# Kernel tuning notes

Measured on AMD Instinct MI355X. Metric: run time of the kernel, lower is better.

## Reference

```python
import jax, jax.numpy as jnp
import numpy as np

N = 200000      # nodes (1000 graphs x 200 nodes)
E = 1600000     # edges
N1 = 100000     # nodes after pool 1
E2 = 100000     # edges of pooled graph
N2 = 50000      # nodes after pool 2
B = 1000        # graphs
F_IN, C1, C2, H, NCLS = 1, 32, 64, 25, 10


def setup_inputs() -> dict:
    key = jax.random.key(0)
    ks = jax.random.split(key, 16)
    def lin(k, i, o):
        return jax.random.normal(k, (i, o), jnp.float32) / np.sqrt(i)
    inp = {
        'x': jax.random.normal(ks[0], (N, F_IN), jnp.float32),
        'pos': jax.random.uniform(ks[1], (N, 2), jnp.float32),
        'edge_index': jax.random.randint(ks[2], (2, E), 0, N, dtype=jnp.int32),
        'edge_attr': jax.random.uniform(ks[3], (E, 2), jnp.float32),
        'batch': (jnp.arange(N, dtype=jnp.int32) // (N // B)),
        'cluster1': (jnp.arange(N, dtype=jnp.int32) // 2),      # pairs of consecutive nodes -> same graph
        'edge_index2': jax.random.randint(ks[4], (2, E2), 0, N1, dtype=jnp.int32),
        'cluster2': (jnp.arange(N1, dtype=jnp.int32) // 2),
        'n1_w1': lin(ks[5], 2, H), 'n1_b1': jnp.zeros((H,), jnp.float32),
        'n1_w2': lin(ks[6], H, F_IN * C1), 'n1_b2': jnp.zeros((F_IN * C1,), jnp.float32),
        'root1': lin(ks[7], F_IN, C1), 'bias1': jnp.zeros((C1,), jnp.float32),
        'n2_w1': lin(ks[8], 2, H), 'n2_b1': jnp.zeros((H,), jnp.float32),
        'n2_w2': lin(ks[9], H, C1 * C2), 'n2_b2': jnp.zeros((C1 * C2,), jnp.float32),
        'root2': lin(ks[10], C1, C2), 'bias2': jnp.zeros((C2,), jnp.float32),
        'fc1_w': lin(ks[11], C2, 128), 'fc1_b': jnp.zeros((128,), jnp.float32),
        'fc2_w': lin(ks[12], 128, NCLS), 'fc2_b': jnp.zeros((NCLS,), jnp.float32),
    }
    return inp


def _cartesian(ei, pos):
    # PyG transforms.Cartesian(norm=True, cat=False)
    cart = pos[ei[0]] - pos[ei[1]]                      # [E, 2]
    m = jnp.max(jnp.abs(cart))
    return cart / (2.0 * m) + 0.5


def _nnconv(x, ei, ea, w1, b1, w2, b2, root, bias, n_nodes, c_in, c_out):
    # edge-conditioned weights: MLP(edge_attr) -> [E, c_in, c_out]
    w = (jax.nn.relu(ea @ w1 + b1) @ w2 + b2).reshape(-1, c_in, c_out)
    msg = jnp.einsum('ei,eio->eo', x[ei[0]], w)          # per-edge matmul with gathered src feats
    agg = jax.ops.segment_sum(msg, ei[1], num_segments=n_nodes)
    return agg + x @ root + bias


def _segment_mean(v, seg, n):
    s = jax.ops.segment_sum(v, seg, num_segments=n)
    c = jax.ops.segment_sum(jnp.ones((v.shape[0], 1), v.dtype), seg, num_segments=n)
    return s / jnp.maximum(c, 1.0)


def reference(x, pos, edge_index, edge_attr, batch, cluster1, edge_index2, cluster2,
              n1_w1, n1_b1, n1_w2, n1_b2, root1, bias1,
              n2_w1, n2_b1, n2_w2, n2_b2, root2, bias2,
              fc1_w, fc1_b, fc2_w, fc2_b):
    h = jax.nn.elu(_nnconv(x, edge_index, edge_attr, n1_w1, n1_b1, n1_w2, n1_b2,
                           root1, bias1, N, F_IN, C1))
    # max_pool(cluster1): segment-max feats, mean pos, carry batch; recompute Cartesian attrs
    x1 = jax.ops.segment_max(h, cluster1, num_segments=N1)
    pos1 = _segment_mean(pos, cluster1, N1)
    batch1 = jax.ops.segment_max(batch, cluster1, num_segments=N1)
    ea2 = _cartesian(edge_index2, pos1)
    h2 = jax.nn.elu(_nnconv(x1, edge_index2, ea2, n2_w1, n2_b1, n2_w2, n2_b2,
                            root2, bias2, N1, C1, C2))
    # max_pool_x(cluster2)
    x2 = jax.ops.segment_max(h2, cluster2, num_segments=N2)
    batch2 = jax.ops.segment_max(batch1, cluster2, num_segments=N2)
    g = _segment_mean(x2, batch2, B)                    # global_mean_pool -> [B, 64]
    z = jax.nn.elu(g @ fc1_w + fc1_b)                   # dropout is identity in eval
    return jax.nn.log_softmax(z @ fc2_w + fc2_b, axis=1)
```

## Files before the change

kernel.cpp:

```cpp
#include <hip/hip_runtime.h>
#include <hip/hip_bf16.h>

#define N_NODES 200000
#define E1 1600000
#define N1P 100000
#define E2P 100000
#define N2P 50000
#define BGR 1000
#define C1 32
#define C2 64
#define HIDN 25
#define NCLS 10

typedef short short8 __attribute__((ext_vector_type(8)));
typedef int int4v __attribute__((ext_vector_type(4)));
typedef float f32x4 __attribute__((ext_vector_type(4)));
typedef float f32x2 __attribute__((ext_vector_type(2)));

union FragU { int4v i; short8 s; };

__device__ __forceinline__ float elu1(float v) {
    return v > 0.f ? v : expm1f(v);
}
__device__ __forceinline__ float bf2f(unsigned short u) {
    return __uint_as_float(((unsigned int)u) << 16);
}
__device__ __forceinline__ unsigned int pk_bf16(float a, float b) {
    unsigned int r;
    asm("v_cvt_pk_bf16_f32 %0, %1, %2" : "=v"(r) : "v"(a), "v"(b));
    return r;
}
__device__ __forceinline__ void atomic_pk_bf16(unsigned short* p, unsigned int pk) {
    asm volatile("global_atomic_pk_add_bf16 %0, %1, off" :: "v"(p), "v"(pk) : "memory");
}

__global__ __launch_bounds__(256) void bgbuild1_kernel(
    const float* __restrict__ w2, const float* __restrict__ b2,
    unsigned int* __restrict__ W2f)
{
    int q = blockIdx.x * 256 + threadIdx.x;
    if (q >= 512) return;
    int jj = q & 3, l = (q >> 2) & 63, m = q >> 8;
    int k0 = (l >> 4) * 8 + 2 * jj;
    int o = 2 * (l & 15) + m;
    float v0 = (k0 < 25) ? w2[k0 * 32 + o] : (k0 == 25 ? b2[o] : 0.f);
    int k1 = k0 + 1;
    float v1 = (k1 < 25) ? w2[k1 * 32 + o] : (k1 == 25 ? b2[o] : 0.f);
    W2f[q] = pk_bf16(v0, v1);
}

__global__ __launch_bounds__(256) void conv1_kernel(
    const float* __restrict__ x, const float* __restrict__ ea,
    const int* __restrict__ ei,
    const float* __restrict__ w1, const float* __restrict__ b1,
    const unsigned int* __restrict__ W2f,
    unsigned short* __restrict__ agg1b)
{
    __shared__ unsigned int afrag[16][4][64];
    __shared__ int dst_lds[256];

    int t = threadIdx.x;
    int e = blockIdx.x * 256 + t;
    f32x2 a = ((const f32x2*)ea)[e];
    int s = ei[e], d = ei[E1 + e];
    float xv = x[s];
    dst_lds[t] = d;

    float v[26];
#pragma unroll
    for (int h = 0; h < HIDN; ++h) {
        float u = fmaf(a.x, w1[h], fmaf(a.y, w1[HIDN + h], b1[h]));
        v[h] = fmaxf(u, 0.f) * xv;
    }
    v[25] = xv;

    int tile = t >> 4, r = t & 15;
#pragma unroll
    for (int p = 0; p < 13; ++p) {
        int g = p >> 2, j = p & 3;
        afrag[tile][j][g * 16 + r] = pk_bf16(v[2 * p], v[2 * p + 1]);
    }
    afrag[tile][1][48 + r] = 0;
    afrag[tile][2][48 + r] = 0;
    afrag[tile][3][48 + r] = 0;
    __syncthreads();

    int lane = t & 63, wave = t >> 6;
    FragU bf0, bf1;
    bf0.i = *(const int4v*)(W2f + lane * 4);
    bf1.i = *(const int4v*)(W2f + (64 + lane) * 4);
    int c = lane & 15, rg = lane >> 4;

#pragma unroll
    for (int ti = 0; ti < 4; ++ti) {
        int tl = wave * 4 + ti;
        FragU af;
        af.i.x = afrag[tl][0][lane];
        af.i.y = afrag[tl][1][lane];
        af.i.z = afrag[tl][2][lane];
        af.i.w = afrag[tl][3][lane];
        f32x4 a0 = (f32x4){0.f, 0.f, 0.f, 0.f};
        f32x4 a1 = (f32x4){0.f, 0.f, 0.f, 0.f};
        a0 = __builtin_amdgcn_mfma_f32_16x16x32_bf16(af.s, bf0.s, a0, 0, 0, 0);
        a1 = __builtin_amdgcn_mfma_f32_16x16x32_bf16(af.s, bf1.s, a1, 0, 0, 0);
#pragma unroll
        for (int jj = 0; jj < 4; ++jj) {
            int le = tl * 16 + rg * 4 + jj;
            atomic_pk_bf16(agg1b + (size_t)dst_lds[le] * C1 + 2 * c,
                           pk_bf16(a0[jj], a1[jj]));
        }
    }
}

__global__ __launch_bounds__(256) void pool1_kernel(
    const unsigned short* __restrict__ agg1b, const float* __restrict__ x,
    const float* __restrict__ root1, const float* __restrict__ bias1,
    const float* __restrict__ pos, unsigned short* __restrict__ x1b,
    float* __restrict__ pos1)
{
    int t = blockIdx.x * blockDim.x + threadIdx.x;
    if (t >= N1P * C1) return;
    int j = t >> 5, o = t & 31;
    int na = 2 * j, nb = 2 * j + 1;
    float r = root1[o], bo = bias1[o];
    float ha = elu1(bf2f(agg1b[(size_t)na * C1 + o]) + x[na] * r + bo);
    float hb = elu1(bf2f(agg1b[(size_t)nb * C1 + o]) + x[nb] * r + bo);
    float mx = fmaxf(ha, hb);
    x1b[t] = (unsigned short)(pk_bf16(mx, mx) & 0xffffu);
    if (o < 2) pos1[j * 2 + o] = 0.5f * (pos[na * 2 + o] + pos[nb * 2 + o]);
}

__global__ __launch_bounds__(256) void maxabs_kernel(
    const int* __restrict__ ei2, const float* __restrict__ pos1,
    unsigned int* __restrict__ maxbits)
{
    int e = blockIdx.x * blockDim.x + threadIdx.x;
    float m = 0.f;
    if (e < E2P) {
        int s = ei2[e], d = ei2[E2P + e];
        float c0 = pos1[2 * s] - pos1[2 * d];
        float c1 = pos1[2 * s + 1] - pos1[2 * d + 1];
        m = fmaxf(fabsf(c0), fabsf(c1));
    }
#pragma unroll
    for (int off = 32; off; off >>= 1)
        m = fmaxf(m, __shfl_down(m, off));
    if ((threadIdx.x & 63) == 0)
        atomicMax(maxbits, __float_as_uint(m));
}

__global__ __launch_bounds__(256) void bgbuild_kernel(
    const float* __restrict__ w2, const float* __restrict__ b2,
    unsigned int* __restrict__ Bg)
{
    int idx = blockIdx.x * 256 + threadIdx.x;
    if (idx >= 26 * 4 * 64 * 4) return;
    int g0 = idx * 2;
    int j = g0 & 7;
    int l = (g0 >> 3) & 63;
    int nb = (g0 >> 9) & 3;
    int kt = g0 >> 11;
    int k = kt * 32 + (l >> 4) * 8 + j;
    int o = (nb >> 1) * 32 + 2 * (l & 15) + (nb & 1);
    float v0, v1;
    if (k < 800) { v0 = w2[k * 64 + o]; v1 = w2[(k + 1) * 64 + o]; }
    else         { v0 = b2[(k - 800) * 64 + o]; v1 = b2[(k - 799) * 64 + o]; }
    Bg[idx] = pk_bf16(v0, v1);
}

__global__ __launch_bounds__(256) void conv2_kernel(
    const int* __restrict__ ei2, const float* __restrict__ pos1,
    const unsigned short* __restrict__ x1b,
    const float* __restrict__ w1, const float* __restrict__ b1,
    const unsigned int* __restrict__ maxbits,
    const unsigned int* __restrict__ Bg,
    unsigned short* __restrict__ agg2b)
{
    __shared__ __align__(16) unsigned short xs_lds[256][40];
    __shared__ float hid_lds[256][27];
    __shared__ int dst_lds[256];

    int t = threadIdx.x;
    int ge = blockIdx.x * 256 + t;

    {
        float inv = 0.5f / __uint_as_float(maxbits[0]);
        int s = 0, d = 0;
        if (ge < E2P) { s = ei2[ge]; d = ei2[E2P + ge]; }
        dst_lds[t] = d;
        float a0 = (pos1[2 * s] - pos1[2 * d]) * inv + 0.5f;
        float a1 = (pos1[2 * s + 1] - pos1[2 * d + 1]) * inv + 0.5f;
#pragma unroll
        for (int h = 0; h < HIDN; ++h) {
            float u = fmaf(a0, w1[h], fmaf(a1, w1[HIDN + h], b1[h]));
            hid_lds[t][h] = fmaxf(u, 0.f);
        }
        const int4v* xp = (const int4v*)(x1b + (size_t)s * C1);
#pragma unroll
        for (int q = 0; q < 4; ++q)
            *(int4v*)&xs_lds[t][q * 8] = xp[q];
    }
    __syncthreads();

    int lane = t & 63, wave = t >> 6;
    int c = lane & 15, rg = lane >> 4;

    FragU xv4[4];
    float xfl[4][8];
#pragma unroll
    for (int ti = 0; ti < 4; ++ti) {
        int row = (wave * 4 + ti) * 16 + c;
        xv4[ti].i = *(const int4v*)&xs_lds[row][rg * 8];
#pragma unroll
        for (int g2 = 0; g2 < 4; ++g2) {
            unsigned int u = (unsigned int)xv4[ti].i[g2];
            xfl[ti][2 * g2]     = __uint_as_float(u << 16);
            xfl[ti][2 * g2 + 1] = __uint_as_float(u & 0xffff0000u);
        }
    }

    f32x4 acc[4][4];
#pragma unroll
    for (int ti = 0; ti < 4; ++ti)
#pragma unroll
        for (int nb = 0; nb < 4; ++nb)
            acc[ti][nb] = (f32x4){0.f, 0.f, 0.f, 0.f};

    const int4v* Bg4 = (const int4v*)Bg;
#pragma unroll 2
    for (int kt = 0; kt < 25; ++kt) {
        FragU bf[4];
#pragma unroll
        for (int nb = 0; nb < 4; ++nb)
            bf[nb].i = Bg4[(kt * 4 + nb) * 64 + lane];
#pragma unroll
        for (int ti = 0; ti < 4; ++ti) {
            float hv = hid_lds[(wave * 4 + ti) * 16 + c][kt];
            FragU af;
            af.i.x = pk_bf16(hv * xfl[ti][0], hv * xfl[ti][1]);
            af.i.y = pk_bf16(hv * xfl[ti][2], hv * xfl[ti][3]);
            af.i.z = pk_bf16(hv * xfl[ti][4], hv * xfl[ti][5]);
            af.i.w = pk_bf16(hv * xfl[ti][6], hv * xfl[ti][7]);
#pragma unroll
            for (int nb = 0; nb < 4; ++nb)
                acc[ti][nb] = __builtin_amdgcn_mfma_f32_16x16x32_bf16(af.s, bf[nb].s, acc[ti][nb], 0, 0, 0);
        }
    }
    {
        FragU bf[4];
#pragma unroll
        for (int nb = 0; nb < 4; ++nb)
            bf[nb].i = Bg4[(25 * 4 + nb) * 64 + lane];
#pragma unroll
        for (int ti = 0; ti < 4; ++ti)
#pragma unroll
            for (int nb = 0; nb < 4; ++nb)
                acc[ti][nb] = __builtin_amdgcn_mfma_f32_16x16x32_bf16(xv4[ti].s, bf[nb].s, acc[ti][nb], 0, 0, 0);
    }

#pragma unroll
    for (int ti = 0; ti < 4; ++ti) {
        int tl = wave * 4 + ti;
#pragma unroll
        for (int jj = 0; jj < 4; ++jj) {
            int le = tl * 16 + rg * 4 + jj;
            if (blockIdx.x * 256 + le < E2P) {
                unsigned short* dp = agg2b + (size_t)dst_lds[le] * C2;
                atomic_pk_bf16(dp + 2 * c,      pk_bf16(acc[ti][0][jj], acc[ti][1][jj]));
                atomic_pk_bf16(dp + 32 + 2 * c, pk_bf16(acc[ti][2][jj], acc[ti][3][jj]));
            }
        }
    }
}

__global__ __launch_bounds__(256) void pool2_kernel(
    const unsigned short* __restrict__ agg2b, const unsigned short* __restrict__ x1b,
    const float* __restrict__ root2, const float* __restrict__ bias2,
    float* __restrict__ g)
{
    int b = blockIdx.x;
    int w = threadIdx.x >> 6, o = threadIdx.x & 63;
    __shared__ float part[4][C2];
    float sum = 0.f;
    for (int jj = w; jj < 50; jj += 4) {
        int j = b * 50 + jj;
        float hv[2];
#pragma unroll
        for (int t = 0; t < 2; ++t) {
            int n = 2 * j + t;
            float a = bf2f(agg2b[(size_t)n * C2 + o]) + bias2[o];
#pragma unroll
            for (int i = 0; i < C1; ++i)
                a = fmaf(bf2f(x1b[(size_t)n * C1 + i]), root2[i * C2 + o], a);
            hv[t] = elu1(a);
        }
        sum += fmaxf(hv[0], hv[1]);
    }
    part[w][o] = sum;
    __syncthreads();
    if (w == 0) {
        float s2 = part[0][o] + part[1][o] + part[2][o] + part[3][o];
        g[b * C2 + o] = s2 * (1.f / 50.f);
    }
}

__global__ __launch_bounds__(128) void head_kernel(
    const float* __restrict__ g,
    const float* __restrict__ fc1w, const float* __restrict__ fc1b,
    const float* __restrict__ fc2w, const float* __restrict__ fc2b,
    float* __restrict__ out)
{
    int b = blockIdx.x;
    int t = threadIdx.x;
    __shared__ float gs[C2];
    __shared__ float zs[128];
    __shared__ float ls[NCLS];
    if (t < C2) gs[t] = g[b * C2 + t];
    __syncthreads();
    float z = fc1b[t];
#pragma unroll
    for (int i = 0; i < C2; ++i) z = fmaf(gs[i], fc1w[i * 128 + t], z);
    zs[t] = elu1(z);
    __syncthreads();
    if (t < NCLS) {
        float l = fc2b[t];
#pragma unroll
        for (int k = 0; k < 128; ++k) l = fmaf(zs[k], fc2w[k * NCLS + t], l);
        ls[t] = l;
    }
    __syncthreads();
    if (t < NCLS) {
        float mx = ls[0];
#pragma unroll
        for (int c = 1; c < NCLS; ++c) mx = fmaxf(mx, ls[c]);
        float se = 0.f;
#pragma unroll
        for (int c = 0; c < NCLS; ++c) se += expf(ls[c] - mx);
        out[b * NCLS + t] = ls[t] - mx - logf(se);
    }
}

extern "C" void kernel_launch(void* const* d_in, const int* in_sizes, int n_in,
                              void* d_out, int out_size, void* d_ws, size_t ws_size,
                              hipStream_t stream)
{
    const float* x    = (const float*)d_in[0];
    const float* pos  = (const float*)d_in[1];
    const int*   ei   = (const int*)d_in[2];
    const float* ea   = (const float*)d_in[3];
    const int*   ei2  = (const int*)d_in[6];
    const float* n1w1 = (const float*)d_in[8];
    const float* n1b1 = (const float*)d_in[9];
    const float* n1w2 = (const float*)d_in[10];
    const float* n1b2 = (const float*)d_in[11];
    const float* root1= (const float*)d_in[12];
    const float* bias1= (const float*)d_in[13];
    const float* n2w1 = (const float*)d_in[14];
    const float* n2b1 = (const float*)d_in[15];
    const float* n2w2 = (const float*)d_in[16];
    const float* n2b2 = (const float*)d_in[17];
    const float* root2= (const float*)d_in[18];
    const float* bias2= (const float*)d_in[19];
    const float* fc1w = (const float*)d_in[20];
    const float* fc1b = (const float*)d_in[21];
    const float* fc2w = (const float*)d_in[22];
    const float* fc2b = (const float*)d_in[23];
    float* out = (float*)d_out;

    char* w = (char*)d_ws;
    unsigned short* agg1b = (unsigned short*)w;  w += (size_t)N_NODES * C1 * 2;
    unsigned short* x1b   = (unsigned short*)w;  w += (size_t)N1P * C1 * 2;
    float* pos1 = (float*)w;                     w += (size_t)N1P * 2 * 4;
    unsigned int* maxbits = (unsigned int*)w;    w += 256;
    unsigned short* agg2b = (unsigned short*)w;  w += (size_t)N1P * C2 * 2;
    float* g    = (float*)w;                     w += (size_t)BGR * C2 * 4;
    unsigned int* Bg = (unsigned int*)w;         w += 26624 * 4;
    unsigned int* W2f = (unsigned int*)w;        w += 512 * 4;

    hipMemsetAsync(agg1b, 0, (size_t)N_NODES * C1 * 2, stream);
    hipMemsetAsync(agg2b, 0, (size_t)N1P * C2 * 2, stream);
    hipMemsetAsync(maxbits, 0, 256, stream);

    bgbuild1_kernel<<<2, 256, 0, stream>>>(n1w2, n1b2, W2f);
    bgbuild_kernel<<<104, 256, 0, stream>>>(n2w2, n2b2, Bg);
    conv1_kernel<<<E1 / 256, 256, 0, stream>>>(x, ea, ei, n1w1, n1b1, W2f, agg1b);
    pool1_kernel<<<(N1P * C1 + 255) / 256, 256, 0, stream>>>(agg1b, x, root1, bias1, pos, x1b, pos1);
    maxabs_kernel<<<(E2P + 255) / 256, 256, 0, stream>>>(ei2, pos1, maxbits);
    conv2_kernel<<<(E2P + 255) / 256, 256, 0, stream>>>(ei2, pos1, x1b, n2w1, n2b1, maxbits, Bg, agg2b);
    pool2_kernel<<<BGR, 256, 0, stream>>>(agg2b, x1b, root2, bias2, g);
    head_kernel<<<BGR, 128, 0, stream>>>(g, fc1w, fc1b, fc2w, fc2b, out);
}
```

Measured before the change: 188.1 us.

## Merge weight-build kernels, fuse pool2 with head, halve conv2 tile size

```diff
diff --git a/kernel.cpp b/kernel.cpp
--- a/kernel.cpp
+++ b/kernel.cpp
@@ -34,19 +34,36 @@
     asm volatile("global_atomic_pk_add_bf16 %0, %1, off" :: "v"(p), "v"(pk) : "memory");
 }
 
-__global__ __launch_bounds__(256) void bgbuild1_kernel(
-    const float* __restrict__ w2, const float* __restrict__ b2,
-    unsigned int* __restrict__ W2f)
-{
-    int q = blockIdx.x * 256 + threadIdx.x;
-    if (q >= 512) return;
-    int jj = q & 3, l = (q >> 2) & 63, m = q >> 8;
-    int k0 = (l >> 4) * 8 + 2 * jj;
-    int o = 2 * (l & 15) + m;
-    float v0 = (k0 < 25) ? w2[k0 * 32 + o] : (k0 == 25 ? b2[o] : 0.f);
-    int k1 = k0 + 1;
-    float v1 = (k1 < 25) ? w2[k1 * 32 + o] : (k1 == 25 ? b2[o] : 0.f);
-    W2f[q] = pk_bf16(v0, v1);
+__global__ __launch_bounds__(256) void bgbuild_kernel(
+    const float* __restrict__ w2a, const float* __restrict__ b2a,
+    const float* __restrict__ w2b, const float* __restrict__ b2b,
+    unsigned int* __restrict__ W2f, unsigned int* __restrict__ Bg)
+{
+    int blk = blockIdx.x, t = threadIdx.x;
+    if (blk < 2) {
+        int q = blk * 256 + t;
+        int jj = q & 3, l = (q >> 2) & 63, m = q >> 8;
+        int k0 = (l >> 4) * 8 + 2 * jj;
+        int o = 2 * (l & 15) + m;
+        float v0 = (k0 < 25) ? w2a[k0 * 32 + o] : (k0 == 25 ? b2a[o] : 0.f);
+        int k1 = k0 + 1;
+        float v1 = (k1 < 25) ? w2a[k1 * 32 + o] : (k1 == 25 ? b2a[o] : 0.f);
+        W2f[q] = pk_bf16(v0, v1);
+    } else {
+        int idx = (blk - 2) * 256 + t;
+        if (idx >= 26 * 4 * 64 * 4) return;
+        int g0 = idx * 2;
+        int j = g0 & 7;
+        int l = (g0 >> 3) & 63;
+        int nb = (g0 >> 9) & 3;
+        int kt = g0 >> 11;
+        int k = kt * 32 + (l >> 4) * 8 + j;
+        int o = (nb >> 1) * 32 + 2 * (l & 15) + (nb & 1);
+        float v0, v1;
+        if (k < 800) { v0 = w2b[k * 64 + o]; v1 = w2b[(k + 1) * 64 + o]; }
+        else         { v0 = b2b[(k - 800) * 64 + o]; v1 = b2b[(k - 799) * 64 + o]; }
+        Bg[idx] = pk_bf16(v0, v1);
+    }
 }
 
 __global__ __launch_bounds__(256) void conv1_kernel(
@@ -74,15 +91,15 @@
     }
     v[25] = xv;
 
-    int tile = t >> 4, r = t & 15;
+    int tile = t >> 4, r16 = t & 15;
 #pragma unroll
     for (int p = 0; p < 13; ++p) {
         int g = p >> 2, j = p & 3;
-        afrag[tile][j][g * 16 + r] = pk_bf16(v[2 * p], v[2 * p + 1]);
-    }
-    afrag[tile][1][48 + r] = 0;
-    afrag[tile][2][48 + r] = 0;
-    afrag[tile][3][48 + r] = 0;
+        afrag[tile][j][g * 16 + r16] = pk_bf16(v[2 * p], v[2 * p + 1]);
+    }
+    afrag[tile][1][48 + r16] = 0;
+    afrag[tile][2][48 + r16] = 0;
+    afrag[tile][3][48 + r16] = 0;
     __syncthreads();
 
     int lane = t & 63, wave = t >> 6;
@@ -149,25 +166,6 @@
         atomicMax(maxbits, __float_as_uint(m));
 }
 
-__global__ __launch_bounds__(256) void bgbuild_kernel(
-    const float* __restrict__ w2, const float* __restrict__ b2,
-    unsigned int* __restrict__ Bg)
-{
-    int idx = blockIdx.x * 256 + threadIdx.x;
-    if (idx >= 26 * 4 * 64 * 4) return;
-    int g0 = idx * 2;
-    int j = g0 & 7;
-    int l = (g0 >> 3) & 63;
-    int nb = (g0 >> 9) & 3;
-    int kt = g0 >> 11;
-    int k = kt * 32 + (l >> 4) * 8 + j;
-    int o = (nb >> 1) * 32 + 2 * (l & 15) + (nb & 1);
-    float v0, v1;
-    if (k < 800) { v0 = w2[k * 64 + o]; v1 = w2[(k + 1) * 64 + o]; }
-    else         { v0 = b2[(k - 800) * 64 + o]; v1 = b2[(k - 799) * 64 + o]; }
-    Bg[idx] = pk_bf16(v0, v1);
-}
-
 __global__ __launch_bounds__(256) void conv2_kernel(
     const int* __restrict__ ei2, const float* __restrict__ pos1,
     const unsigned short* __restrict__ x1b,
@@ -176,95 +174,106 @@
     const unsigned int* __restrict__ Bg,
     unsigned short* __restrict__ agg2b)
 {
-    __shared__ __align__(16) unsigned short xs_lds[256][40];
-    __shared__ float hid_lds[256][27];
-    __shared__ int dst_lds[256];
+    __shared__ __align__(16) unsigned short xs_lds[128][40];
+    __shared__ unsigned int hidb[128][14];
+    __shared__ int dst_lds[128];
 
     int t = threadIdx.x;
-    int ge = blockIdx.x * 256 + t;
-
-    {
+    int base = blockIdx.x * 128;
+
+    if (t < 128) {
+        int ge = base + t;
+        bool ok = ge < E2P;
         float inv = 0.5f / __uint_as_float(maxbits[0]);
         int s = 0, d = 0;
-        if (ge < E2P) { s = ei2[ge]; d = ei2[E2P + ge]; }
+        if (ok) { s = ei2[ge]; d = ei2[E2P + ge]; }
         dst_lds[t] = d;
         float a0 = (pos1[2 * s] - pos1[2 * d]) * inv + 0.5f;
         float a1 = (pos1[2 * s + 1] - pos1[2 * d + 1]) * inv + 0.5f;
+        float hv[26];
 #pragma unroll
         for (int h = 0; h < HIDN; ++h) {
             float u = fmaf(a0, w1[h], fmaf(a1, w1[HIDN + h], b1[h]));
-            hid_lds[t][h] = fmaxf(u, 0.f);
-        }
+            hv[h] = ok ? fmaxf(u, 0.f) : 0.f;
+        }
+        hv[25] = 0.f;
+#pragma unroll
+        for (int p = 0; p < 13; ++p)
+            hidb[t][p] = pk_bf16(hv[2 * p], hv[2 * p + 1]);
         const int4v* xp = (const int4v*)(x1b + (size_t)s * C1);
 #pragma unroll
-        for (int q = 0; q < 4; ++q)
-            *(int4v*)&xs_lds[t][q * 8] = xp[q];
+        for (int q = 0; q < 4; ++q) {
+            int4v z4 = (int4v){0, 0, 0, 0};
+            *(int4v*)&xs_lds[t][q * 8] = ok ? xp[q] : z4;
+        }
     }
     __syncthreads();
 
     int lane = t & 63, wave = t >> 6;
     int c = lane & 15, rg = lane >> 4;
 
-    FragU xv4[4];
-    float xfl[4][8];
-#pragma unroll
-    for (int ti = 0; ti < 4; ++ti) {
-        int row = (wave * 4 + ti) * 16 + c;
-        xv4[ti].i = *(const int4v*)&xs_lds[row][rg * 8];
+    FragU xv2[2];
+    float xfl[2][8];
+#pragma unroll
+    for (int ti = 0; ti < 2; ++ti) {
+        int row = (wave * 2 + ti) * 16 + c;
+        xv2[ti].i = *(const int4v*)&xs_lds[row][rg * 8];
 #pragma unroll
         for (int g2 = 0; g2 < 4; ++g2) {
-            unsigned int u = (unsigned int)xv4[ti].i[g2];
+            unsigned int u = (unsigned int)xv2[ti].i[g2];
             xfl[ti][2 * g2]     = __uint_as_float(u << 16);
             xfl[ti][2 * g2 + 1] = __uint_as_float(u & 0xffff0000u);
         }
     }
 
-    f32x4 acc[4][4];
-#pragma unroll
-    for (int ti = 0; ti < 4; ++ti)
+    f32x4 acc[2][4];
+#pragma unroll
+    for (int ti = 0; ti < 2; ++ti)
 #pragma unroll
         for (int nb = 0; nb < 4; ++nb)
             acc[ti][nb] = (f32x4){0.f, 0.f, 0.f, 0.f};
 
     const int4v* Bg4 = (const int4v*)Bg;
-#pragma unroll 2
+    FragU bf[4];
+#pragma unroll
+    for (int nb = 0; nb < 4; ++nb)
+        bf[nb].i = Bg4[nb * 64 + lane];
+
+#pragma unroll
     for (int kt = 0; kt < 25; ++kt) {
-        FragU bf[4];
+        FragU bn[4];
 #pragma unroll
         for (int nb = 0; nb < 4; ++nb)
-            bf[nb].i = Bg4[(kt * 4 + nb) * 64 + lane];
-#pragma unroll
-        for (int ti = 0; ti < 4; ++ti) {
-            float hv = hid_lds[(wave * 4 + ti) * 16 + c][kt];
+            bn[nb].i = Bg4[((kt + 1) * 4 + nb) * 64 + lane];
+#pragma unroll
+        for (int ti = 0; ti < 2; ++ti) {
+            unsigned int hu = hidb[(wave * 2 + ti) * 16 + c][kt >> 1];
+            float hvv = bf2f((unsigned short)((kt & 1) ? (hu >> 16) : (hu & 0xffffu)));
             FragU af;
-            af.i.x = pk_bf16(hv * xfl[ti][0], hv * xfl[ti][1]);
-            af.i.y = pk_bf16(hv * xfl[ti][2], hv * xfl[ti][3]);
-            af.i.z = pk_bf16(hv * xfl[ti][4], hv * xfl[ti][5]);
-            af.i.w = pk_bf16(hv * xfl[ti][6], hv * xfl[ti][7]);
+            af.i.x = pk_bf16(hvv * xfl[ti][0], hvv * xfl[ti][1]);
+            af.i.y = pk_bf16(hvv * xfl[ti][2], hvv * xfl[ti][3]);
+            af.i.z = pk_bf16(hvv * xfl[ti][4], hvv * xfl[ti][5]);
+            af.i.w = pk_bf16(hvv * xfl[ti][6], hvv * xfl[ti][7]);
 #pragma unroll
             for (int nb = 0; nb < 4; ++nb)
                 acc[ti][nb] = __builtin_amdgcn_mfma_f32_16x16x32_bf16(af.s, bf[nb].s, acc[ti][nb], 0, 0, 0);
         }
-    }
-    {
-        FragU bf[4];
+#pragma unroll
+        for (int nb = 0; nb < 4; ++nb) bf[nb] = bn[nb];
+    }
+#pragma unroll
+    for (int ti = 0; ti < 2; ++ti)
 #pragma unroll
         for (int nb = 0; nb < 4; ++nb)
-            bf[nb].i = Bg4[(25 * 4 + nb) * 64 + lane];
-#pragma unroll
-        for (int ti = 0; ti < 4; ++ti)
-#pragma unroll
-            for (int nb = 0; nb < 4; ++nb)
-                acc[ti][nb] = __builtin_amdgcn_mfma_f32_16x16x32_bf16(xv4[ti].s, bf[nb].s, acc[ti][nb], 0, 0, 0);
-    }
-
-#pragma unroll
-    for (int ti = 0; ti < 4; ++ti) {
-        int tl = wave * 4 + ti;
+            acc[ti][nb] = __builtin_amdgcn_mfma_f32_16x16x32_bf16(xv2[ti].s, bf[nb].s, acc[ti][nb], 0, 0, 0);
+
+#pragma unroll
+    for (int ti = 0; ti < 2; ++ti) {
+        int tl = wave * 2 + ti;
 #pragma unroll
         for (int jj = 0; jj < 4; ++jj) {
             int le = tl * 16 + rg * 4 + jj;
-            if (blockIdx.x * 256 + le < E2P) {
+            if (base + le < E2P) {
                 unsigned short* dp = agg2b + (size_t)dst_lds[le] * C2;
                 atomic_pk_bf16(dp + 2 * c,      pk_bf16(acc[ti][0][jj], acc[ti][1][jj]));
                 atomic_pk_bf16(dp + 32 + 2 * c, pk_bf16(acc[ti][2][jj], acc[ti][3][jj]));
@@ -273,54 +282,47 @@
     }
 }
 
-__global__ __launch_bounds__(256) void pool2_kernel(
+__global__ __launch_bounds__(256) void pool2_head_kernel(
     const unsigned short* __restrict__ agg2b, const unsigned short* __restrict__ x1b,
     const float* __restrict__ root2, const float* __restrict__ bias2,
-    float* __restrict__ g)
+    const float* __restrict__ fc1w, const float* __restrict__ fc1b,
+    const float* __restrict__ fc2w, const float* __restrict__ fc2b,
+    float* __restrict__ out)
 {
     int b = blockIdx.x;
-    int w = threadIdx.x >> 6, o = threadIdx.x & 63;
+    int t = threadIdx.x;
+    int w = t >> 6, o = t & 63;
     __shared__ float part[4][C2];
+    __shared__ float gs[C2];
+    __shared__ float zs[128];
+    __shared__ float ls[NCLS];
+
     float sum = 0.f;
     for (int jj = w; jj < 50; jj += 4) {
         int j = b * 50 + jj;
         float hv[2];
 #pragma unroll
-        for (int t = 0; t < 2; ++t) {
-            int n = 2 * j + t;
+        for (int tt = 0; tt < 2; ++tt) {
+            int n = 2 * j + tt;
             float a = bf2f(agg2b[(size_t)n * C2 + o]) + bias2[o];
 #pragma unroll
             for (int i = 0; i < C1; ++i)
                 a = fmaf(bf2f(x1b[(size_t)n * C1 + i]), root2[i * C2 + o], a);
-            hv[t] = elu1(a);
+            hv[tt] = elu1(a);
         }
         sum += fmaxf(hv[0], hv[1]);
     }
     part[w][o] = sum;
     __syncthreads();
-    if (w == 0) {
-        float s2 = part[0][o] + part[1][o] + part[2][o] + part[3][o];
-        g[b * C2 + o] = s2 * (1.f / 50.f);
-    }
-}
-
-__global__ __launch_bounds__(128) void head_kernel(
-    const float* __restrict__ g,
-    const float* __restrict__ fc1w, const float* __restrict__ fc1b,
-    const float* __restrict__ fc2w, const float* __restrict__ fc2b,
-    float* __restrict__ out)
-{
-    int b = blockIdx.x;
-    int t = threadIdx.x;
-    __shared__ float gs[C2];
-    __shared__ float zs[128];
-    __shared__ float ls[NCLS];
-    if (t < C2) gs[t] = g[b * C2 + t];
-    __syncthreads();
-    float z = fc1b[t];
-#pragma unroll
-    for (int i = 0; i < C2; ++i) z = fmaf(gs[i], fc1w[i * 128 + t], z);
-    zs[t] = elu1(z);
+    if (w == 0)
+        gs[o] = (part[0][o] + part[1][o] + part[2][o] + part[3][o]) * (1.f / 50.f);
+    __syncthreads();
+    if (t < 128) {
+        float z = fc1b[t];
+#pragma unroll
+        for (int i = 0; i < C2; ++i) z = fmaf(gs[i], fc1w[i * 128 + t], z);
+        zs[t] = elu1(z);
+    }
     __syncthreads();
     if (t < NCLS) {
         float l = fc2b[t];
@@ -332,10 +334,10 @@
     if (t < NCLS) {
         float mx = ls[0];
 #pragma unroll
-        for (int c = 1; c < NCLS; ++c) mx = fmaxf(mx, ls[c]);
+        for (int cc = 1; cc < NCLS; ++cc) mx = fmaxf(mx, ls[cc]);
         float se = 0.f;
 #pragma unroll
-        for (int c = 0; c < NCLS; ++c) se += expf(ls[c] - mx);
+        for (int cc = 0; cc < NCLS; ++cc) se += expf(ls[cc] - mx);
         out[b * NCLS + t] = ls[t] - mx - logf(se);
     }
 }
@@ -373,7 +375,6 @@
     float* pos1 = (float*)w;                     w += (size_t)N1P * 2 * 4;
     unsigned int* maxbits = (unsigned int*)w;    w += 256;
     unsigned short* agg2b = (unsigned short*)w;  w += (size_t)N1P * C2 * 2;
-    float* g    = (float*)w;                     w += (size_t)BGR * C2 * 4;
     unsigned int* Bg = (unsigned int*)w;         w += 26624 * 4;
     unsigned int* W2f = (unsigned int*)w;        w += 512 * 4;
 
@@ -381,12 +382,11 @@
     hipMemsetAsync(agg2b, 0, (size_t)N1P * C2 * 2, stream);
     hipMemsetAsync(maxbits, 0, 256, stream);
 
-    bgbuild1_kernel<<<2, 256, 0, stream>>>(n1w2, n1b2, W2f);
-    bgbuild_kernel<<<104, 256, 0, stream>>>(n2w2, n2b2, Bg);
+    bgbuild_kernel<<<106, 256, 0, stream>>>(n1w2, n1b2, n2w2, n2b2, W2f, Bg);
     conv1_kernel<<<E1 / 256, 256, 0, stream>>>(x, ea, ei, n1w1, n1b1, W2f, agg1b);
     pool1_kernel<<<(N1P * C1 + 255) / 256, 256, 0, stream>>>(agg1b, x, root1, bias1, pos, x1b, pos1);
     maxabs_kernel<<<(E2P + 255) / 256, 256, 0, stream>>>(ei2, pos1, maxbits);
-    conv2_kernel<<<(E2P + 255) / 256, 256, 0, stream>>>(ei2, pos1, x1b, n2w1, n2b1, maxbits, Bg, agg2b);
-    pool2_kernel<<<BGR, 256, 0, stream>>>(agg2b, x1b, root2, bias2, g);
-    head_kernel<<<BGR, 128, 0, stream>>>(g, fc1w, fc1b, fc2w, fc2b, out);
-}
+    conv2_kernel<<<(E2P + 127) / 128, 256, 0, stream>>>(ei2, pos1, x1b, n2w1, n2b1, maxbits, Bg, agg2b);
+    pool2_head_kernel<<<BGR, 256, 0, stream>>>(agg2b, x1b, root2, bias2,
+                                               fc1w, fc1b, fc2w, fc2b, out);
+}
```

Result: no change. 186.5 us (-0.9%).
